# Optimization experiments

Measured on AMD Instinct MI355X. Metric: run time of the kernel, lower is better.

Reference implementation:

```python
import jax, jax.numpy as jnp
import numpy as np

B, S, E, H, D = 2, 2048, 512, 8, 64
NEG = -1e10


def setup_inputs() -> dict:
    key = jax.random.key(0)
    k1, k2, k3, k4, k5, k6 = jax.random.split(key, 6)
    inputs = jax.random.normal(k1, (B, S, E), dtype=jnp.float32)
    keys = jax.random.normal(k2, (B, S, H, D), dtype=jnp.float32)
    values = jax.random.normal(k3, (B, S, H, D), dtype=jnp.float32)
    # xavier-uniform style scale for square weights
    lim = float(np.sqrt(6.0 / (E + H * D)))
    query_weights = jax.random.uniform(k4, (E, H * D), minval=-lim, maxval=lim, dtype=jnp.float32)
    output_weights = jax.random.uniform(k5, (H * D, E), minval=-lim, maxval=lim, dtype=jnp.float32)
    mask = jax.random.randint(k6, (B, S, S), 0, 2).astype(jnp.bool_)
    return {"inputs": inputs, "keys": keys, "values": values,
            "query_weights": query_weights, "output_weights": output_weights,
            "mask": mask}


def reference(inputs, keys, values, query_weights, output_weights, mask):
    # project queries: (B,S,E) @ (E,H*D) -> (B,S,H,D)
    q = jnp.matmul(inputs, query_weights).reshape(B, S, H, D)
    # scores: (B,H,Sq,Sk)
    scores = jnp.einsum('bqhd,bkhd->bhqk', q, keys) / jnp.sqrt(jnp.float32(D))
    # masked_fill(mask, -1e10); mask broadcasts over heads
    scores = jnp.where(mask[:, None, :, :], jnp.float32(NEG), scores)
    probs = jax.nn.softmax(scores, axis=-1)
    # (B,H,Sq,Sk) x (B,Sk,H,D) -> (B,Sq,H,D)
    out = jnp.einsum('bhqk,bkhd->bqhd', probs, values)
    out = out.reshape(B, S, H * D)
    return jnp.matmul(out, output_weights)
```

## Files before the change

### kernel.cpp

```cpp
#include <hip/hip_runtime.h>
#include <hip/hip_bf16.h>

namespace {

constexpr int B = 2, S = 2048, E = 512, H = 8, D = 64, HD = 512;
constexpr float SL = 0.125f * 1.44269504f;
constexpr int PLD = 40;

typedef __attribute__((ext_vector_type(8))) short bf16x8;
typedef __attribute__((ext_vector_type(4))) unsigned short u16x4;
typedef __attribute__((ext_vector_type(4))) float f32x4;
typedef __attribute__((ext_vector_type(4))) float float4v;

__device__ __forceinline__ ushort f2b(float x) {
  __hip_bfloat16 h = __float2bfloat16(x);
  return *reinterpret_cast<const ushort*>(&h);
}

__global__ __launch_bounds__(256) void prep_fused_kernel(
    const float* __restrict__ K, const float* __restrict__ V,
    const float* __restrict__ Wq, const float* __restrict__ Wo,
    const int* __restrict__ maskp,
    ushort* __restrict__ Kbf, ushort* __restrict__ Vtbf,
    ushort* __restrict__ Wtq, ushort* __restrict__ Wto,
    uint4* __restrict__ keep4) {
  const int bid = blockIdx.x;
  const int t = threadIdx.x;
  if (bid < 512) {
    __shared__ __align__(16) ushort Vn[64][76];
    const int kt = bid & 31;
    const int bh = bid >> 5;
    const int b = bh >> 3, h = bh & 7;
    const int k0 = kt * 64;
#pragma unroll
    for (int i = 0; i < 4; ++i) {
      int c = i * 256 + t;
      int kk = c >> 4, d4 = (c & 15) * 4;
      size_t g = ((size_t)(b * 2048 + k0 + kk) * 8 + h) * 64 + d4;
      float4v kv = *(const float4v*)(K + g);
      float4v vv = *(const float4v*)(V + g);
      u16x4 kp = {f2b(kv.x), f2b(kv.y), f2b(kv.z), f2b(kv.w)};
      u16x4 vp = {f2b(vv.x), f2b(vv.y), f2b(vv.z), f2b(vv.w)};
      *(u16x4*)(Kbf + ((size_t)(bh * 2048 + k0 + kk)) * 64 + d4) = kp;
      *(u16x4*)&Vn[kk][d4] = vp;
    }
    __syncthreads();
#pragma unroll
    for (int i = 0; i < 2; ++i) {
      int c = i * 256 + t;
      int kc8 = (c & 7) * 8, d = c >> 3;
      union { ushort u[8]; bf16x8 v; } p;
#pragma unroll
      for (int j = 0; j < 8; ++j) p.u[j] = Vn[kc8 + j][d];
      *(bf16x8*)(Vtbf + ((size_t)(bh * 64 + d)) * 2048 + k0 + kc8) = p.v;
    }
  } else if (bid < 640) {
    __shared__ __align__(16) ushort T[64][68];
    const int idx = bid - 512;
    const float* Wsrc = (idx >> 6) ? Wo : Wq;
    ushort* Wdst = (idx >> 6) ? Wto : Wtq;
    const int x = idx & 63;
    const int k0 = (x & 7) * 64, n0 = (x >> 3) * 64;
#pragma unroll
    for (int i = 0; i < 4; ++i) {
      int c = i * 256 + t;
      int kk = c >> 4, n4 = (c & 15) * 4;
      float4v v = *(const float4v*)(Wsrc + (size_t)(k0 + kk) * 512 + n0 + n4);
      u16x4 p = {f2b(v.x), f2b(v.y), f2b(v.z), f2b(v.w)};
      *(u16x4*)&T[kk][n4] = p;
    }
    __syncthreads();
#pragma unroll
    for (int i = 0; i < 2; ++i) {
      int c = i * 256 + t;
      int n = c >> 3, k8 = (c & 7) * 8;
      union { ushort u[8]; bf16x8 v; } p;
#pragma unroll
      for (int j = 0; j < 8; ++j) p.u[j] = T[k8 + j][n];
      *(bf16x8*)(Wdst + (size_t)(n0 + n) * 512 + k0 + k8) = p.v;
    }
  } else {
    const int wid = (bid - 640) * 4 + (t >> 6);
    const int row = wid >> 3, c = wid & 7;
    const int lane = t & 63;
    const int4 v = *((const int4*)(maskp + (size_t)row * 2048 + c * 256) + lane);
    unsigned long long bx = __ballot(v.x == 0);
    unsigned long long by = __ballot(v.y == 0);
    unsigned long long bz = __ballot(v.z == 0);
    unsigned long long bw = __ballot(v.w == 0);
    if (lane == 0)
      keep4[(size_t)row * 16 + c * 2] = uint4{(uint)bx, (uint)by, (uint)bz, (uint)bw};
    if (lane == 32)
      keep4[(size_t)row * 16 + c * 2 + 1] =
          uint4{(uint)(bx >> 32), (uint)(by >> 32), (uint)(bz >> 32), (uint)(bw >> 32)};
  }
}

__global__ __launch_bounds__(256) void proj_out_kernel(
    const ushort* __restrict__ A, const ushort* __restrict__ Wt, float* __restrict__ C) {
  __shared__ __align__(16) ushort As[64][PLD];
  __shared__ __align__(16) ushort Ws[64][PLD];

  const int tid = threadIdx.x;
  const int lane = tid & 63;
  const int w = tid >> 6;
  const int col = lane & 15;
  const int quad = lane >> 4;
  const int m0 = blockIdx.y * 64;
  const int n0 = blockIdx.x * 64;
  const int wm = (w & 1) * 32;
  const int wn = (w >> 1) * 32;
  const int ar = tid >> 2;
  const int ak = (tid & 3) * 8;
  const int wn2 = tid >> 2;
  const int wkc = (tid & 3) * 8;

  f32x4 acc[2][2];
#pragma unroll
  for (int i = 0; i < 2; ++i)
#pragma unroll
    for (int j = 0; j < 2; ++j) acc[i][j] = f32x4{0.f, 0.f, 0.f, 0.f};

  const ushort* Ap = A + (size_t)(m0 + ar) * 512 + ak;
  const ushort* Wp = Wt + (size_t)(n0 + wn2) * 512 + wkc;
  bf16x8 apre = *(const bf16x8*)Ap;
  bf16x8 wp = *(const bf16x8*)Wp;

  for (int kt = 0; kt < 16; ++kt) {
    if (kt) __syncthreads();
    *(bf16x8*)&As[ar][ak] = apre;
    *(bf16x8*)&Ws[wn2][wkc] = wp;
    if (kt < 15) {
      const int k1 = (kt + 1) * 32;
      apre = *(const bf16x8*)(Ap + k1);
      wp = *(const bf16x8*)(Wp + k1);
    }
    __syncthreads();

    bf16x8 ah[2], wb[2];
#pragma unroll
    for (int i = 0; i < 2; ++i)
      ah[i] = *(const bf16x8*)&As[wm + i * 16 + col][quad * 8];
#pragma unroll
    for (int j = 0; j < 2; ++j)
      wb[j] = *(const bf16x8*)&Ws[wn + j * 16 + col][quad * 8];
#pragma unroll
    for (int i = 0; i < 2; ++i)
#pragma unroll
      for (int j = 0; j < 2; ++j)
        acc[i][j] = __builtin_amdgcn_mfma_f32_16x16x32_bf16(ah[i], wb[j], acc[i][j], 0, 0, 0);
  }

#pragma unroll
  for (int i = 0; i < 2; ++i)
#pragma unroll
    for (int j = 0; j < 2; ++j)
#pragma unroll
      for (int r = 0; r < 4; ++r)
        C[(size_t)(m0 + wm + i * 16 + (quad << 2) + r) * 512 + n0 + wn + j * 16 + col] =
            acc[i][j][r];
}

__global__ __launch_bounds__(256) void flash_attn_kernel(
    const float* __restrict__ inp, const ushort* __restrict__ Wtq,
    const ushort* __restrict__ Kbf, const ushort* __restrict__ Vtbf,
    const uint4* __restrict__ keep4, ushort* __restrict__ Op) {
  __shared__ __align__(16) ushort Ks[128][72];
  __shared__ __align__(16) ushort Vt[64][136];
  __shared__ __align__(16) ushort PQ[64][72];

  const int bid = blockIdx.x;
  const int qt = bid & 31;
  const int bh = bid >> 5;
  const int b = bh >> 3, h = bh & 7;
  const int q0 = qt * 64;
  const int tid = threadIdx.x, lane = tid & 63, w = tid >> 6;
  const int col = lane & 15, quad = lane >> 4, quad4 = quad * 4;
  const int wm = (w & 1) * 32;
  const int wn = (w >> 1) * 32;

  {
    const int ar = tid >> 2;
    const int ak = (tid & 3) * 8;

    f32x4 qacc[2][2];
#pragma unroll
    for (int i = 0; i < 2; ++i)
#pragma unroll
      for (int j = 0; j < 2; ++j) qacc[i][j] = f32x4{0.f, 0.f, 0.f, 0.f};

    const float* Ap = inp + (size_t)(b * 2048 + q0 + ar) * 512 + ak;
    const ushort* Wp = Wtq + (size_t)(h * 64 + ar) * 512 + ak;
    float4v a0p = *(const float4v*)Ap;
    float4v a1p = *(const float4v*)(Ap + 4);
    bf16x8 wp = *(const bf16x8*)Wp;

    for (int kt = 0; kt < 16; ++kt) {
      if (kt) __syncthreads();
      {
        union { ushort u[8]; bf16x8 v; } ap;
        ap.u[0] = f2b(a0p.x); ap.u[1] = f2b(a0p.y); ap.u[2] = f2b(a0p.z); ap.u[3] = f2b(a0p.w);
        ap.u[4] = f2b(a1p.x); ap.u[5] = f2b(a1p.y); ap.u[6] = f2b(a1p.z); ap.u[7] = f2b(a1p.w);
        *(bf16x8*)&PQ[ar][ak] = ap.v;
        *(bf16x8*)&PQ[ar][40 + ak] = wp;
      }
      if (kt < 15) {
        const int k1 = (kt + 1) * 32;
        a0p = *(const float4v*)(Ap + k1);
        a1p = *(const float4v*)(Ap + k1 + 4);
        wp = *(const bf16x8*)(Wp + k1);
      }
      __syncthreads();

      bf16x8 ah[2], wb[2];
#pragma unroll
      for (int i = 0; i < 2; ++i)
        ah[i] = *(const bf16x8*)&PQ[wm + i * 16 + col][quad * 8];
#pragma unroll
      for (int j = 0; j < 2; ++j)
        wb[j] = *(const bf16x8*)&PQ[wn + j * 16 + col][40 + quad * 8];
#pragma unroll
      for (int i = 0; i < 2; ++i)
#pragma unroll
        for (int j = 0; j < 2; ++j)
          qacc[i][j] = __builtin_amdgcn_mfma_f32_16x16x32_bf16(ah[i], wb[j], qacc[i][j], 0, 0, 0);
    }

    __syncthreads();
#pragma unroll
    for (int i = 0; i < 2; ++i)
#pragma unroll
      for (int j = 0; j < 2; ++j)
#pragma unroll
        for (int r = 0; r < 4; ++r)
          PQ[wm + i * 16 + quad4 + r][wn + j * 16 + col] = f2b(qacc[i][j][r]);
    __syncthreads();
  }

  const bf16x8 qb0 = *(const bf16x8*)&PQ[w * 16 + col][quad * 8];
  const bf16x8 qb1 = *(const bf16x8*)&PQ[w * 16 + col][32 + quad * 8];

  f32x4 oacc[4];
#pragma unroll
  for (int c = 0; c < 4; ++c) oacc[c] = f32x4{0.f, 0.f, 0.f, 0.f};
  f32x4 lacc = f32x4{0.f, 0.f, 0.f, 0.f};

  union { ushort u[8]; bf16x8 v; } onesu;
#pragma unroll
  for (int j = 0; j < 8; ++j) onesu.u[j] = 0x3F80;
  const bf16x8 onesB = onesu.v;

  const uint4* kr = keep4 + (size_t)(b * 2048 + q0 + w * 16 + col) * 16;
  const ushort* Kbase = Kbf + (size_t)bh * 2048 * 64;
  const ushort* Vbase = Vtbf + (size_t)bh * 64 * 2048;

  bf16x8 kpre[4], vpre[4];
  uint4 kw = kr[0];
#pragma unroll
  for (int i = 0; i < 4; ++i) {
    int c = i * 256 + tid;
    kpre[i] = *(const bf16x8*)(Kbase + (size_t)c * 8);
    int d = c >> 4, k8 = (c & 15) * 8;
    vpre[i] = *(const bf16x8*)(Vbase + (size_t)d * 2048 + k8);
  }

  for (int kt = 0; kt < 16; ++kt) {
    if (kt) __syncthreads();
#pragma unroll
    for (int i = 0; i < 4; ++i) {
      int c = i * 256 + tid;
      *(bf16x8*)&Ks[c >> 3][(c & 7) * 8] = kpre[i];
      int d = c >> 4, k8 = (c & 15) * 8;
      *(bf16x8*)&Vt[d][k8] = vpre[i];
    }
    uint4 kwn = kw;
    if (kt < 15) {
      const int k1 = (kt + 1) * 128;
      kwn = kr[kt + 1];
#pragma unroll
      for (int i = 0; i < 4; ++i) {
        int c = i * 256 + tid;
        kpre[i] = *(const bf16x8*)(Kbase + (size_t)k1 * 64 + c * 8);
        int d = c >> 4, k8 = (c & 15) * 8;
        vpre[i] = *(const bf16x8*)(Vbase + (size_t)d * 2048 + k1 + k8);
      }
    }
    __syncthreads();

    f32x4 sc[8];
#pragma unroll
    for (int t = 0; t < 8; ++t) sc[t] = f32x4{0.f, 0.f, 0.f, 0.f};
#pragma unroll
    for (int t = 0; t < 8; ++t) {
      bf16x8 ka0 = *(const bf16x8*)&Ks[t * 16 + col][quad * 8];
      bf16x8 ka1 = *(const bf16x8*)&Ks[t * 16 + col][32 + quad * 8];
      sc[t] = __builtin_amdgcn_mfma_f32_16x16x32_bf16(ka0, qb0, sc[t], 0, 0, 0);
      sc[t] = __builtin_amdgcn_mfma_f32_16x16x32_bf16(ka1, qb1, sc[t], 0, 0, 0);
    }

    const uint mx_ = kw.x >> quad, my_ = kw.y >> quad, mz_ = kw.z >> quad, mw_ = kw.w >> quad;
    uint X0[8], X1[8];
#pragma unroll
    for (int t = 0; t < 8; ++t) {
      const int sh = 4 * t;
      float p0 = ((mx_ >> sh) & 1u) ? exp2f(sc[t][0] * SL) : 0.f;
      float p1 = ((my_ >> sh) & 1u) ? exp2f(sc[t][1] * SL) : 0.f;
      float p2 = ((mz_ >> sh) & 1u) ? exp2f(sc[t][2] * SL) : 0.f;
      float p3 = ((mw_ >> sh) & 1u) ? exp2f(sc[t][3] * SL) : 0.f;
      __hip_bfloat162 lo = __float22bfloat162_rn(float2{p0, p1});
      __hip_bfloat162 hi = __float22bfloat162_rn(float2{p2, p3});
      X0[t] = *reinterpret_cast<uint*>(&lo);
      X1[t] = *reinterpret_cast<uint*>(&hi);
    }

#pragma unroll
    for (int kb = 0; kb < 4; ++kb) {
      auto a32 = __builtin_amdgcn_permlane32_swap(X0[2 * kb], X0[2 * kb + 1], false, false);
      auto a16 = __builtin_amdgcn_permlane16_swap(a32[0], a32[1], false, false);
      auto b32 = __builtin_amdgcn_permlane32_swap(X1[2 * kb], X1[2 * kb + 1], false, false);
      auto b16 = __builtin_amdgcn_permlane16_swap(b32[0], b32[1], false, false);
      union { uint u[4]; bf16x8 v; } pu;
      pu.u[0] = a16[0]; pu.u[1] = b16[0]; pu.u[2] = a16[1]; pu.u[3] = b16[1];
      const bf16x8 pa = pu.v;
      lacc = __builtin_amdgcn_mfma_f32_16x16x32_bf16(pa, onesB, lacc, 0, 0, 0);
#pragma unroll
      for (int c = 0; c < 4; ++c) {
        bf16x8 vb = *(const bf16x8*)&Vt[c * 16 + col][kb * 32 + quad * 8];
        oacc[c] = __builtin_amdgcn_mfma_f32_16x16x32_bf16(pa, vb, oacc[c], 0, 0, 0);
      }
    }
    kw = kwn;
  }

  float invO[4];
#pragma unroll
  for (int r = 0; r < 4; ++r) invO[r] = 1.f / lacc[r];
#pragma unroll
  for (int c = 0; c < 4; ++c)
#pragma unroll
    for (int r = 0; r < 4; ++r)
      Op[(size_t)(b * S + q0 + w * 16 + quad4 + r) * HD + h * D + c * 16 + col] =
          f2b(oacc[c][r] * invO[r]);
}

}

extern "C" void kernel_launch(void* const* d_in, const int* in_sizes, int n_in,
                              void* d_out, int out_size, void* d_ws, size_t ws_size,
                              hipStream_t stream) {
  const float* inputs = (const float*)d_in[0];
  const float* keys   = (const float*)d_in[1];
  const float* values = (const float*)d_in[2];
  const float* wq     = (const float*)d_in[3];
  const float* wo     = (const float*)d_in[4];
  const int*   maskp  = (const int*)d_in[5];
  float* out = (float*)d_out;

  ushort* Kbf  = (ushort*)d_out;
  ushort* Vtbf = Kbf + (size_t)2097152;

  char* ws = (char*)d_ws;
  ushort* attnb = (ushort*)ws;
  uint4*  keep4 = (uint4*)(ws + (4 << 20));
  ushort* Wtq   = (ushort*)(ws + (5 << 20));
  ushort* Wto   = (ushort*)(ws + (5 << 20) + (512 << 10));

  dim3 blk(256);
  prep_fused_kernel<<<dim3(8832), blk, 0, stream>>>(keys, values, wq, wo, maskp,
                                                    Kbf, Vtbf, Wtq, Wto, keep4);
  flash_attn_kernel<<<dim3(512), blk, 0, stream>>>(inputs, Wtq, Kbf, Vtbf, keep4, attnb);
  proj_out_kernel<<<dim3(8, 64), blk, 0, stream>>>(attnb, Wto, out);
}
```

Measured before the change: 164.0 us.

## Load K/V fragments straight to registers and widen attention blocks to 128 queries

```diff
diff --git a/kernel.cpp b/kernel.cpp
--- a/kernel.cpp
+++ b/kernel.cpp
@@ -161,27 +161,26 @@
             acc[i][j][r];
 }
 
-__global__ __launch_bounds__(256) void flash_attn_kernel(
+__global__ __launch_bounds__(512, 2) void flash_attn_kernel(
     const float* __restrict__ inp, const ushort* __restrict__ Wtq,
     const ushort* __restrict__ Kbf, const ushort* __restrict__ Vtbf,
     const uint4* __restrict__ keep4, ushort* __restrict__ Op) {
-  __shared__ __align__(16) ushort Ks[128][72];
-  __shared__ __align__(16) ushort Vt[64][136];
-  __shared__ __align__(16) ushort PQ[64][72];
+  __shared__ __align__(16) ushort PQ[128][72];
 
   const int bid = blockIdx.x;
-  const int qt = bid & 31;
-  const int bh = bid >> 5;
+  const int qt = bid & 15;
+  const int bh = bid >> 4;
   const int b = bh >> 3, h = bh & 7;
-  const int q0 = qt * 64;
+  const int q0 = qt * 128;
   const int tid = threadIdx.x, lane = tid & 63, w = tid >> 6;
   const int col = lane & 15, quad = lane >> 4, quad4 = quad * 4;
-  const int wm = (w & 1) * 32;
-  const int wn = (w >> 1) * 32;
+  const int wm = (w & 3) * 32;
+  const int wn = (w >> 2) * 32;
 
   {
     const int ar = tid >> 2;
     const int ak = (tid & 3) * 8;
+    const bool wstage = tid < 256;
 
     f32x4 qacc[2][2];
 #pragma unroll
@@ -193,7 +192,8 @@
     const ushort* Wp = Wtq + (size_t)(h * 64 + ar) * 512 + ak;
     float4v a0p = *(const float4v*)Ap;
     float4v a1p = *(const float4v*)(Ap + 4);
-    bf16x8 wp = *(const bf16x8*)Wp;
+    bf16x8 wp{};
+    if (wstage) wp = *(const bf16x8*)Wp;
 
     for (int kt = 0; kt < 16; ++kt) {
       if (kt) __syncthreads();
@@ -202,13 +202,13 @@
         ap.u[0] = f2b(a0p.x); ap.u[1] = f2b(a0p.y); ap.u[2] = f2b(a0p.z); ap.u[3] = f2b(a0p.w);
         ap.u[4] = f2b(a1p.x); ap.u[5] = f2b(a1p.y); ap.u[6] = f2b(a1p.z); ap.u[7] = f2b(a1p.w);
         *(bf16x8*)&PQ[ar][ak] = ap.v;
-        *(bf16x8*)&PQ[ar][40 + ak] = wp;
+        if (wstage) *(bf16x8*)&PQ[ar][40 + ak] = wp;
       }
       if (kt < 15) {
         const int k1 = (kt + 1) * 32;
         a0p = *(const float4v*)(Ap + k1);
         a1p = *(const float4v*)(Ap + k1 + 4);
-        wp = *(const bf16x8*)(Wp + k1);
+        if (wstage) wp = *(const bf16x8*)(Wp + k1);
       }
       __syncthreads();
 
@@ -251,83 +251,96 @@
   const bf16x8 onesB = onesu.v;
 
   const uint4* kr = keep4 + (size_t)(b * 2048 + q0 + w * 16 + col) * 16;
-  const ushort* Kbase = Kbf + (size_t)bh * 2048 * 64;
-  const ushort* Vbase = Vtbf + (size_t)bh * 64 * 2048;
-
-  bf16x8 kpre[4], vpre[4];
+  const ushort* Kb2 = Kbf + (size_t)bh * 2048 * 64;
+  const ushort* Vb2 = Vtbf + (size_t)bh * 64 * 2048;
+
+  const int ko = col * 64 + quad * 8;
+  const int vo = col * 2048 + quad * 8;
+
+  bf16x8 kf0[8], kf1[8], vf[4][4];
   uint4 kw = kr[0];
 #pragma unroll
-  for (int i = 0; i < 4; ++i) {
-    int c = i * 256 + tid;
-    kpre[i] = *(const bf16x8*)(Kbase + (size_t)c * 8);
-    int d = c >> 4, k8 = (c & 15) * 8;
-    vpre[i] = *(const bf16x8*)(Vbase + (size_t)d * 2048 + k8);
-  }
-
+  for (int t = 0; t < 8; ++t) {
+    kf0[t] = *(const bf16x8*)(Kb2 + ko + t * 1024);
+    kf1[t] = *(const bf16x8*)(Kb2 + ko + t * 1024 + 32);
+  }
+#pragma unroll
+  for (int kb = 0; kb < 4; ++kb)
+#pragma unroll
+    for (int c = 0; c < 4; ++c)
+      vf[kb][c] = *(const bf16x8*)(Vb2 + vo + c * 32768 + kb * 32);
+
+#pragma unroll 1
   for (int kt = 0; kt < 16; ++kt) {
-    if (kt) __syncthreads();
-#pragma unroll
-    for (int i = 0; i < 4; ++i) {
-      int c = i * 256 + tid;
-      *(bf16x8*)&Ks[c >> 3][(c & 7) * 8] = kpre[i];
-      int d = c >> 4, k8 = (c & 15) * 8;
-      *(bf16x8*)&Vt[d][k8] = vpre[i];
-    }
+    __builtin_amdgcn_s_barrier();
+
     uint4 kwn = kw;
+    if (kt < 15) kwn = kr[kt + 1];
+
+    f32x4 sc[8];
+#pragma unroll
+    for (int t = 0; t < 8; ++t) sc[t] = f32x4{0.f, 0.f, 0.f, 0.f};
+#pragma unroll
+    for (int t = 0; t < 8; ++t) {
+      sc[t] = __builtin_amdgcn_mfma_f32_16x16x32_bf16(kf0[t], qb0, sc[t], 0, 0, 0);
+      sc[t] = __builtin_amdgcn_mfma_f32_16x16x32_bf16(kf1[t], qb1, sc[t], 0, 0, 0);
+    }
+
     if (kt < 15) {
-      const int k1 = (kt + 1) * 128;
-      kwn = kr[kt + 1];
-#pragma unroll
-      for (int i = 0; i < 4; ++i) {
-        int c = i * 256 + tid;
-        kpre[i] = *(const bf16x8*)(Kbase + (size_t)k1 * 64 + c * 8);
-        int d = c >> 4, k8 = (c & 15) * 8;
-        vpre[i] = *(const bf16x8*)(Vbase + (size_t)d * 2048 + k1 + k8);
-      }
-    }
-    __syncthreads();
-
-    f32x4 sc[8];
-#pragma unroll
-    for (int t = 0; t < 8; ++t) sc[t] = f32x4{0.f, 0.f, 0.f, 0.f};
-#pragma unroll
-    for (int t = 0; t < 8; ++t) {
-      bf16x8 ka0 = *(const bf16x8*)&Ks[t * 16 + col][quad * 8];
-      bf16x8 ka1 = *(const bf16x8*)&Ks[t * 16 + col][32 + quad * 8];
-      sc[t] = __builtin_amdgcn_mfma_f32_16x16x32_bf16(ka0, qb0, sc[t], 0, 0, 0);
-      sc[t] = __builtin_amdgcn_mfma_f32_16x16x32_bf16(ka1, qb1, sc[t], 0, 0, 0);
+      const ushort* Kn = Kb2 + (kt + 1) * 8192;
+#pragma unroll
+      for (int t = 0; t < 8; ++t) {
+        kf0[t] = *(const bf16x8*)(Kn + ko + t * 1024);
+        kf1[t] = *(const bf16x8*)(Kn + ko + t * 1024 + 32);
+      }
     }
 
     const uint mx_ = kw.x >> quad, my_ = kw.y >> quad, mz_ = kw.z >> quad, mw_ = kw.w >> quad;
-    uint X0[8], X1[8];
-#pragma unroll
-    for (int t = 0; t < 8; ++t) {
-      const int sh = 4 * t;
-      float p0 = ((mx_ >> sh) & 1u) ? exp2f(sc[t][0] * SL) : 0.f;
-      float p1 = ((my_ >> sh) & 1u) ? exp2f(sc[t][1] * SL) : 0.f;
-      float p2 = ((mz_ >> sh) & 1u) ? exp2f(sc[t][2] * SL) : 0.f;
-      float p3 = ((mw_ >> sh) & 1u) ? exp2f(sc[t][3] * SL) : 0.f;
-      __hip_bfloat162 lo = __float22bfloat162_rn(float2{p0, p1});
-      __hip_bfloat162 hi = __float22bfloat162_rn(float2{p2, p3});
-      X0[t] = *reinterpret_cast<uint*>(&lo);
-      X1[t] = *reinterpret_cast<uint*>(&hi);
-    }
-
 #pragma unroll
     for (int kb = 0; kb < 4; ++kb) {
-      auto a32 = __builtin_amdgcn_permlane32_swap(X0[2 * kb], X0[2 * kb + 1], false, false);
+      uint Xa0, Xa1, Xb0, Xb1;
+      {
+        const int sh = 8 * kb;
+        float p0 = ((mx_ >> sh) & 1u) ? exp2f(sc[2 * kb][0] * SL) : 0.f;
+        float p1 = ((my_ >> sh) & 1u) ? exp2f(sc[2 * kb][1] * SL) : 0.f;
+        float p2 = ((mz_ >> sh) & 1u) ? exp2f(sc[2 * kb][2] * SL) : 0.f;
+        float p3 = ((mw_ >> sh) & 1u) ? exp2f(sc[2 * kb][3] * SL) : 0.f;
+        __hip_bfloat162 lo = __float22bfloat162_rn(float2{p0, p1});
+        __hip_bfloat162 hi = __float22bfloat162_rn(float2{p2, p3});
+        Xa0 = *reinterpret_cast<uint*>(&lo);
+        Xa1 = *reinterpret_cast<uint*>(&hi);
+      }
+      {
+        const int sh = 8 * kb + 4;
+        float p0 = ((mx_ >> sh) & 1u) ? exp2f(sc[2 * kb + 1][0] * SL) : 0.f;
+        float p1 = ((my_ >> sh) & 1u) ? exp2f(sc[2 * kb + 1][1] * SL) : 0.f;
+        float p2 = ((mz_ >> sh) & 1u) ? exp2f(sc[2 * kb + 1][2] * SL) : 0.f;
+        float p3 = ((mw_ >> sh) & 1u) ? exp2f(sc[2 * kb + 1][3] * SL) : 0.f;
+        __hip_bfloat162 lo = __float22bfloat162_rn(float2{p0, p1});
+        __hip_bfloat162 hi = __float22bfloat162_rn(float2{p2, p3});
+        Xb0 = *reinterpret_cast<uint*>(&lo);
+        Xb1 = *reinterpret_cast<uint*>(&hi);
+      }
+      auto a32 = __builtin_amdgcn_permlane32_swap(Xa0, Xb0, false, false);
       auto a16 = __builtin_amdgcn_permlane16_swap(a32[0], a32[1], false, false);
-      auto b32 = __builtin_amdgcn_permlane32_swap(X1[2 * kb], X1[2 * kb + 1], false, false);
+      auto b32 = __builtin_amdgcn_permlane32_swap(Xa1, Xb1, false, false);
       auto b16 = __builtin_amdgcn_permlane16_swap(b32[0], b32[1], false, false);
       union { uint u[4]; bf16x8 v; } pu;
       pu.u[0] = a16[0]; pu.u[1] = b16[0]; pu.u[2] = a16[1]; pu.u[3] = b16[1];
       const bf16x8 pa = pu.v;
       lacc = __builtin_amdgcn_mfma_f32_16x16x32_bf16(pa, onesB, lacc, 0, 0, 0);
 #pragma unroll
-      for (int c = 0; c < 4; ++c) {
-        bf16x8 vb = *(const bf16x8*)&Vt[c * 16 + col][kb * 32 + quad * 8];
-        oacc[c] = __builtin_amdgcn_mfma_f32_16x16x32_bf16(pa, vb, oacc[c], 0, 0, 0);
-      }
+      for (int c = 0; c < 4; ++c)
+        oacc[c] = __builtin_amdgcn_mfma_f32_16x16x32_bf16(pa, vf[kb][c], oacc[c], 0, 0, 0);
+    }
+
+    if (kt < 15) {
+      const ushort* Vn = Vb2 + (kt + 1) * 128;
+#pragma unroll
+      for (int kb = 0; kb < 4; ++kb)
+#pragma unroll
+        for (int c = 0; c < 4; ++c)
+          vf[kb][c] = *(const bf16x8*)(Vn + vo + c * 32768 + kb * 32);
     }
     kw = kwn;
   }
@@ -365,9 +378,8 @@
   ushort* Wtq   = (ushort*)(ws + (5 << 20));
   ushort* Wto   = (ushort*)(ws + (5 << 20) + (512 << 10));
 
-  dim3 blk(256);
-  prep_fused_kernel<<<dim3(8832), blk, 0, stream>>>(keys, values, wq, wo, maskp,
-                                                    Kbf, Vtbf, Wtq, Wto, keep4);
-  flash_attn_kernel<<<dim3(512), blk, 0, stream>>>(inputs, Wtq, Kbf, Vtbf, keep4, attnb);
-  proj_out_kernel<<<dim3(8, 64), blk, 0, stream>>>(attnb, Wto, out);
-}
+  prep_fused_kernel<<<dim3(8832), dim3(256), 0, stream>>>(keys, values, wq, wo, maskp,
+                                                          Kbf, Vtbf, Wtq, Wto, keep4);
+  flash_attn_kernel<<<dim3(256), dim3(512), 0, stream>>>(inputs, Wtq, Kbf, Vtbf, keep4, attnb);
+  proj_out_kernel<<<dim3(8, 64), dim3(256), 0, stream>>>(attnb, Wto, out);
+}
```

Result: slower. 236.7 us (+44.3%).

## Split attention key tiles across waves with shared-memory reduction of partial outputs

Applied to the files above, without the earlier changes.

```diff
diff --git a/kernel.cpp b/kernel.cpp
--- a/kernel.cpp
+++ b/kernel.cpp
@@ -161,13 +161,14 @@
             acc[i][j][r];
 }
 
-__global__ __launch_bounds__(256) void flash_attn_kernel(
+__global__ __launch_bounds__(256, 2) void flash_attn_kernel(
     const float* __restrict__ inp, const ushort* __restrict__ Wtq,
     const ushort* __restrict__ Kbf, const ushort* __restrict__ Vtbf,
     const uint4* __restrict__ keep4, ushort* __restrict__ Op) {
-  __shared__ __align__(16) ushort Ks[128][72];
-  __shared__ __align__(16) ushort Vt[64][136];
-  __shared__ __align__(16) ushort PQ[64][72];
+  __shared__ __align__(16) union SM {
+    struct { ushort Ks[128][72]; ushort Vt[64][136]; ushort PQ[64][72]; } m;
+    struct { float red[3][64][68]; float lred[3][64]; } r;
+  } sm;
 
   const int bid = blockIdx.x;
   const int qt = bid & 31;
@@ -201,8 +202,8 @@
         union { ushort u[8]; bf16x8 v; } ap;
         ap.u[0] = f2b(a0p.x); ap.u[1] = f2b(a0p.y); ap.u[2] = f2b(a0p.z); ap.u[3] = f2b(a0p.w);
         ap.u[4] = f2b(a1p.x); ap.u[5] = f2b(a1p.y); ap.u[6] = f2b(a1p.z); ap.u[7] = f2b(a1p.w);
-        *(bf16x8*)&PQ[ar][ak] = ap.v;
-        *(bf16x8*)&PQ[ar][40 + ak] = wp;
+        *(bf16x8*)&sm.m.PQ[ar][ak] = ap.v;
+        *(bf16x8*)&sm.m.PQ[ar][40 + ak] = wp;
       }
       if (kt < 15) {
         const int k1 = (kt + 1) * 32;
@@ -215,10 +216,10 @@
       bf16x8 ah[2], wb[2];
 #pragma unroll
       for (int i = 0; i < 2; ++i)
-        ah[i] = *(const bf16x8*)&PQ[wm + i * 16 + col][quad * 8];
+        ah[i] = *(const bf16x8*)&sm.m.PQ[wm + i * 16 + col][quad * 8];
 #pragma unroll
       for (int j = 0; j < 2; ++j)
-        wb[j] = *(const bf16x8*)&PQ[wn + j * 16 + col][40 + quad * 8];
+        wb[j] = *(const bf16x8*)&sm.m.PQ[wn + j * 16 + col][40 + quad * 8];
 #pragma unroll
       for (int i = 0; i < 2; ++i)
 #pragma unroll
@@ -233,29 +234,37 @@
       for (int j = 0; j < 2; ++j)
 #pragma unroll
         for (int r = 0; r < 4; ++r)
-          PQ[wm + i * 16 + quad4 + r][wn + j * 16 + col] = f2b(qacc[i][j][r]);
-    __syncthreads();
-  }
-
-  const bf16x8 qb0 = *(const bf16x8*)&PQ[w * 16 + col][quad * 8];
-  const bf16x8 qb1 = *(const bf16x8*)&PQ[w * 16 + col][32 + quad * 8];
-
-  f32x4 oacc[4];
-#pragma unroll
-  for (int c = 0; c < 4; ++c) oacc[c] = f32x4{0.f, 0.f, 0.f, 0.f};
-  f32x4 lacc = f32x4{0.f, 0.f, 0.f, 0.f};
+          sm.m.PQ[wm + i * 16 + quad4 + r][wn + j * 16 + col] = f2b(qacc[i][j][r]);
+    __syncthreads();
+  }
+
+  bf16x8 qb[4][2];
+#pragma unroll
+  for (int j = 0; j < 4; ++j)
+#pragma unroll
+    for (int hf = 0; hf < 2; ++hf)
+      qb[j][hf] = *(const bf16x8*)&sm.m.PQ[j * 16 + col][hf * 32 + quad * 8];
+
+  f32x4 oacc[4][4];
+#pragma unroll
+  for (int j = 0; j < 4; ++j)
+#pragma unroll
+    for (int c = 0; c < 4; ++c) oacc[j][c] = f32x4{0.f, 0.f, 0.f, 0.f};
+  f32x4 lacc[4];
+#pragma unroll
+  for (int j = 0; j < 4; ++j) lacc[j] = f32x4{0.f, 0.f, 0.f, 0.f};
 
   union { ushort u[8]; bf16x8 v; } onesu;
 #pragma unroll
   for (int j = 0; j < 8; ++j) onesu.u[j] = 0x3F80;
   const bf16x8 onesB = onesu.v;
 
-  const uint4* kr = keep4 + (size_t)(b * 2048 + q0 + w * 16 + col) * 16;
+  const uint4* kr0 = keep4 + (size_t)(b * 2048 + q0 + col) * 16;
   const ushort* Kbase = Kbf + (size_t)bh * 2048 * 64;
   const ushort* Vbase = Vtbf + (size_t)bh * 64 * 2048;
+  const int mshift = 8 * w + quad;
 
   bf16x8 kpre[4], vpre[4];
-  uint4 kw = kr[0];
 #pragma unroll
   for (int i = 0; i < 4; ++i) {
     int c = i * 256 + tid;
@@ -269,14 +278,15 @@
 #pragma unroll
     for (int i = 0; i < 4; ++i) {
       int c = i * 256 + tid;
-      *(bf16x8*)&Ks[c >> 3][(c & 7) * 8] = kpre[i];
+      *(bf16x8*)&sm.m.Ks[c >> 3][(c & 7) * 8] = kpre[i];
       int d = c >> 4, k8 = (c & 15) * 8;
-      *(bf16x8*)&Vt[d][k8] = vpre[i];
-    }
-    uint4 kwn = kw;
+      *(bf16x8*)&sm.m.Vt[d][k8] = vpre[i];
+    }
+    uint4 kwj[4];
+#pragma unroll
+    for (int j = 0; j < 4; ++j) kwj[j] = kr0[j * 256 + kt];
     if (kt < 15) {
       const int k1 = (kt + 1) * 128;
-      kwn = kr[kt + 1];
 #pragma unroll
       for (int i = 0; i < 4; ++i) {
         int c = i * 256 + tid;
@@ -287,60 +297,122 @@
     }
     __syncthreads();
 
-    f32x4 sc[8];
-#pragma unroll
-    for (int t = 0; t < 8; ++t) sc[t] = f32x4{0.f, 0.f, 0.f, 0.f};
-#pragma unroll
-    for (int t = 0; t < 8; ++t) {
-      bf16x8 ka0 = *(const bf16x8*)&Ks[t * 16 + col][quad * 8];
-      bf16x8 ka1 = *(const bf16x8*)&Ks[t * 16 + col][32 + quad * 8];
-      sc[t] = __builtin_amdgcn_mfma_f32_16x16x32_bf16(ka0, qb0, sc[t], 0, 0, 0);
-      sc[t] = __builtin_amdgcn_mfma_f32_16x16x32_bf16(ka1, qb1, sc[t], 0, 0, 0);
-    }
-
-    const uint mx_ = kw.x >> quad, my_ = kw.y >> quad, mz_ = kw.z >> quad, mw_ = kw.w >> quad;
-    uint X0[8], X1[8];
-#pragma unroll
-    for (int t = 0; t < 8; ++t) {
-      const int sh = 4 * t;
-      float p0 = ((mx_ >> sh) & 1u) ? exp2f(sc[t][0] * SL) : 0.f;
-      float p1 = ((my_ >> sh) & 1u) ? exp2f(sc[t][1] * SL) : 0.f;
-      float p2 = ((mz_ >> sh) & 1u) ? exp2f(sc[t][2] * SL) : 0.f;
-      float p3 = ((mw_ >> sh) & 1u) ? exp2f(sc[t][3] * SL) : 0.f;
-      __hip_bfloat162 lo = __float22bfloat162_rn(float2{p0, p1});
-      __hip_bfloat162 hi = __float22bfloat162_rn(float2{p2, p3});
-      X0[t] = *reinterpret_cast<uint*>(&lo);
-      X1[t] = *reinterpret_cast<uint*>(&hi);
-    }
-
-#pragma unroll
-    for (int kb = 0; kb < 4; ++kb) {
-      auto a32 = __builtin_amdgcn_permlane32_swap(X0[2 * kb], X0[2 * kb + 1], false, false);
+    bf16x8 ka[2][2];
+#pragma unroll
+    for (int t = 0; t < 2; ++t)
+#pragma unroll
+      for (int hf = 0; hf < 2; ++hf)
+        ka[t][hf] = *(const bf16x8*)&sm.m.Ks[w * 32 + t * 16 + col][hf * 32 + quad * 8];
+
+    f32x4 sc[2][4];
+#pragma unroll
+    for (int t = 0; t < 2; ++t)
+#pragma unroll
+      for (int j = 0; j < 4; ++j) sc[t][j] = f32x4{0.f, 0.f, 0.f, 0.f};
+#pragma unroll
+    for (int t = 0; t < 2; ++t)
+#pragma unroll
+      for (int hf = 0; hf < 2; ++hf)
+#pragma unroll
+        for (int j = 0; j < 4; ++j)
+          sc[t][j] = __builtin_amdgcn_mfma_f32_16x16x32_bf16(ka[t][hf], qb[j][hf], sc[t][j], 0, 0, 0);
+
+    bf16x8 vb[4];
+#pragma unroll
+    for (int c = 0; c < 4; ++c)
+      vb[c] = *(const bf16x8*)&sm.m.Vt[c * 16 + col][w * 32 + quad * 8];
+
+#pragma unroll
+    for (int j = 0; j < 4; ++j) {
+      const uint mx_ = kwj[j].x >> mshift, my_ = kwj[j].y >> mshift,
+                 mz_ = kwj[j].z >> mshift, mw_ = kwj[j].w >> mshift;
+      uint Xa0, Xa1, Xb0, Xb1;
+      {
+        float p0 = (mx_ & 1u) ? exp2f(sc[0][j][0] * SL) : 0.f;
+        float p1 = (my_ & 1u) ? exp2f(sc[0][j][1] * SL) : 0.f;
+        float p2 = (mz_ & 1u) ? exp2f(sc[0][j][2] * SL) : 0.f;
+        float p3 = (mw_ & 1u) ? exp2f(sc[0][j][3] * SL) : 0.f;
+        __hip_bfloat162 lo = __float22bfloat162_rn(float2{p0, p1});
+        __hip_bfloat162 hi = __float22bfloat162_rn(float2{p2, p3});
+        Xa0 = *reinterpret_cast<uint*>(&lo);
+        Xa1 = *reinterpret_cast<uint*>(&hi);
+      }
+      {
+        float p0 = ((mx_ >> 4) & 1u) ? exp2f(sc[1][j][0] * SL) : 0.f;
+        float p1 = ((my_ >> 4) & 1u) ? exp2f(sc[1][j][1] * SL) : 0.f;
+        float p2 = ((mz_ >> 4) & 1u) ? exp2f(sc[1][j][2] * SL) : 0.f;
+        float p3 = ((mw_ >> 4) & 1u) ? exp2f(sc[1][j][3] * SL) : 0.f;
+        __hip_bfloat162 lo = __float22bfloat162_rn(float2{p0, p1});
+        __hip_bfloat162 hi = __float22bfloat162_rn(float2{p2, p3});
+        Xb0 = *reinterpret_cast<uint*>(&lo);
+        Xb1 = *reinterpret_cast<uint*>(&hi);
+      }
+      auto a32 = __builtin_amdgcn_permlane32_swap(Xa0, Xb0, false, false);
       auto a16 = __builtin_amdgcn_permlane16_swap(a32[0], a32[1], false, false);
-      auto b32 = __builtin_amdgcn_permlane32_swap(X1[2 * kb], X1[2 * kb + 1], false, false);
+      auto b32 = __builtin_amdgcn_permlane32_swap(Xa1, Xb1, false, false);
       auto b16 = __builtin_amdgcn_permlane16_swap(b32[0], b32[1], false, false);
       union { uint u[4]; bf16x8 v; } pu;
       pu.u[0] = a16[0]; pu.u[1] = b16[0]; pu.u[2] = a16[1]; pu.u[3] = b16[1];
       const bf16x8 pa = pu.v;
-      lacc = __builtin_amdgcn_mfma_f32_16x16x32_bf16(pa, onesB, lacc, 0, 0, 0);
+      lacc[j] = __builtin_amdgcn_mfma_f32_16x16x32_bf16(pa, onesB, lacc[j], 0, 0, 0);
+#pragma unroll
+      for (int c = 0; c < 4; ++c)
+        oacc[j][c] = __builtin_amdgcn_mfma_f32_16x16x32_bf16(pa, vb[c], oacc[j][c], 0, 0, 0);
+    }
+  }
+
+  __syncthreads();
+  if (w > 0) {
+    const int wi = w - 1;
+#pragma unroll
+    for (int j = 0; j < 4; ++j)
+#pragma unroll
+      for (int c = 0; c < 4; ++c)
+        *(f32x4*)&sm.r.red[wi][c * 16 + col][j * 16 + quad4] = oacc[j][c];
+    if (col == 0)
+#pragma unroll
+      for (int j = 0; j < 4; ++j)
+        *(f32x4*)&sm.r.lred[wi][j * 16 + quad4] = lacc[j];
+  }
+  __syncthreads();
+  if (w == 0) {
+#pragma unroll
+    for (int j = 0; j < 4; ++j) {
 #pragma unroll
       for (int c = 0; c < 4; ++c) {
-        bf16x8 vb = *(const bf16x8*)&Vt[c * 16 + col][kb * 32 + quad * 8];
-        oacc[c] = __builtin_amdgcn_mfma_f32_16x16x32_bf16(pa, vb, oacc[c], 0, 0, 0);
-      }
-    }
-    kw = kwn;
-  }
-
-  float invO[4];
-#pragma unroll
-  for (int r = 0; r < 4; ++r) invO[r] = 1.f / lacc[r];
-#pragma unroll
-  for (int c = 0; c < 4; ++c)
-#pragma unroll
-    for (int r = 0; r < 4; ++r)
-      Op[(size_t)(b * S + q0 + w * 16 + quad4 + r) * HD + h * D + c * 16 + col] =
-          f2b(oacc[c][r] * invO[r]);
+        f32x4 s = oacc[j][c];
+#pragma unroll
+        for (int i = 0; i < 3; ++i)
+          s += *(const f32x4*)&sm.r.red[i][c * 16 + col][j * 16 + quad4];
+        oacc[j][c] = s;
+      }
+      f32x4 ls = lacc[j];
+#pragma unroll
+      for (int i = 0; i < 3; ++i)
+        ls += *(const f32x4*)&sm.r.lred[i][j * 16 + quad4];
+      lacc[j] = ls;
+    }
+#pragma unroll
+    for (int j = 0; j < 4; ++j) {
+#pragma unroll
+      for (int c = 0; c < 4; ++c)
+        *(f32x4*)&sm.r.red[0][c * 16 + col][j * 16 + quad4] = oacc[j][c];
+      if (col == 0) *(f32x4*)&sm.r.lred[0][j * 16 + quad4] = lacc[j];
+    }
+  }
+  __syncthreads();
+
+  {
+    const int q = tid >> 2, d0 = (tid & 3) * 16;
+    const float inv = 1.f / sm.r.lred[0][q];
+    union { ushort u[16]; bf16x8 v[2]; } ob;
+#pragma unroll
+    for (int dd = 0; dd < 16; ++dd)
+      ob.u[dd] = f2b(sm.r.red[0][d0 + dd][q] * inv);
+    ushort* dst = Op + (size_t)(b * S + q0 + q) * HD + h * D + d0;
+    *(bf16x8*)dst = ob.v[0];
+    *(bf16x8*)(dst + 8) = ob.v[1];
+  }
 }
 
 }
@@ -365,9 +437,8 @@
   ushort* Wtq   = (ushort*)(ws + (5 << 20));
   ushort* Wto   = (ushort*)(ws + (5 << 20) + (512 << 10));
 
-  dim3 blk(256);
-  prep_fused_kernel<<<dim3(8832), blk, 0, stream>>>(keys, values, wq, wo, maskp,
-                                                    Kbf, Vtbf, Wtq, Wto, keep4);
-  flash_attn_kernel<<<dim3(512), blk, 0, stream>>>(inputs, Wtq, Kbf, Vtbf, keep4, attnb);
-  proj_out_kernel<<<dim3(8, 64), blk, 0, stream>>>(attnb, Wto, out);
-}
+  prep_fused_kernel<<<dim3(8832), dim3(256), 0, stream>>>(keys, values, wq, wo, maskp,
+                                                          Kbf, Vtbf, Wtq, Wto, keep4);
+  flash_attn_kernel<<<dim3(512), dim3(256), 0, stream>>>(inputs, Wtq, Kbf, Vtbf, keep4, attnb);
+  proj_out_kernel<<<dim3(8, 64), dim3(256), 0, stream>>>(attnb, Wto, out);
+}
```

Result: no change. 161.0 us (-1.8%).
